# Kernel tuning notes

Hardware: AMD Instinct MI355X
Metric: run time of the kernel (lower is better)

## Reference

```python
import jax, jax.numpy as jnp
import numpy as np

SEQ, BATCH, IN, H = 2048, 1024, 10, 20


def setup_inputs() -> dict:
    key = jax.random.key(0)
    ks = jax.random.split(key, 11)
    s = 1.0 / np.sqrt(H)  # PyTorch LSTM init range
    u = lambda k, shape: jax.random.uniform(k, shape, jnp.float32, -s, s)
    return {
        "x": jax.random.normal(ks[0], (SEQ, BATCH, IN), jnp.float32),
        "h0": jax.random.normal(ks[1], (2, BATCH, H), jnp.float32),
        "c0": jax.random.normal(ks[2], (2, BATCH, H), jnp.float32),
        "w_ih_f": u(ks[3], (4 * H, IN)),
        "w_hh_f": u(ks[4], (4 * H, H)),
        "b_ih_f": u(ks[5], (4 * H,)),
        "b_hh_f": u(ks[6], (4 * H,)),
        "w_ih_b": u(ks[7], (4 * H, IN)),
        "w_hh_b": u(ks[8], (4 * H, H)),
        "b_ih_b": u(ks[9], (4 * H,)),
        "b_hh_b": u(ks[10], (4 * H,)),
    }


def _scan_dir(x_proj, h0, c0, w_hh):
    # x_proj: [seq, batch, 4H] precomputed input projection + biases
    def step(carry, g_in):
        h, c = carry
        g = g_in + h @ w_hh.T  # [batch, 4H]
        i, f, gg, o = jnp.split(g, 4, axis=-1)  # PyTorch gate order i,f,g,o
        c = jax.nn.sigmoid(f) * c + jax.nn.sigmoid(i) * jnp.tanh(gg)
        h = jax.nn.sigmoid(o) * jnp.tanh(c)
        return (h, c), h

    (hT, cT), hs = jax.lax.scan(step, (h0, c0), x_proj)
    return hs, hT, cT


def reference(x, h0, c0, w_ih_f, w_hh_f, b_ih_f, b_hh_f, w_ih_b, w_hh_b, b_ih_b, b_hh_b):
    # forward direction
    xf = jnp.einsum('sbi,gi->sbg', x, w_ih_f) + (b_ih_f + b_hh_f)
    hs_f, hT_f, cT_f = _scan_dir(xf, h0[0], c0[0], w_hh_f)
    # backward direction: scan over time-reversed sequence, then flip outputs
    xb = jnp.einsum('sbi,gi->sbg', x[::-1], w_ih_b) + (b_ih_b + b_hh_b)
    hs_b, hT_b, cT_b = _scan_dir(xb, h0[1], c0[1], w_hh_b)
    hs_b = hs_b[::-1]
    out = jnp.concatenate([hs_f, hs_b], axis=-1)  # [seq, batch, 2H]
    h_n = jnp.stack([hT_f, hT_b])  # [2, batch, H]
    c_n = jnp.stack([cT_f, cT_b])
    return out, h_n, c_n
```

## Files before the change

### kernel.cpp

```cpp
#include <hip/hip_runtime.h>

namespace {

constexpr int SEQ = 2048, BATCH = 1024, IN = 10, H = 20;
constexpr int XS  = 32;
constexpr int XRW = 8;
constexpr float L2E = 1.4426950408889634f;
constexpr float K2  = -2.0f * L2E;

typedef _Float16 h2t __attribute__((ext_vector_type(2)));

__device__ __forceinline__ float rcpf(float x) { return __builtin_amdgcn_rcpf(x); }
__device__ __forceinline__ float xp2(float x)  { return __builtin_amdgcn_exp2f(x); }

__device__ __forceinline__ int pk(float a, float b) {
    auto v = __builtin_amdgcn_cvt_pkrtz(a, b);
    int i; __builtin_memcpy(&i, &v, 4); return i;
}
__device__ __forceinline__ float dot2(int a, int b, float c) {
    h2t ha, hb; __builtin_memcpy(&ha, &a, 4); __builtin_memcpy(&hb, &b, 4);
    return __builtin_amdgcn_fdot2(ha, hb, c, false);
}
__device__ __forceinline__ float dpp_x1(float v) {
    int i; __builtin_memcpy(&i, &v, 4);
    int r = __builtin_amdgcn_update_dpp(0, i, 0xB1, 0xF, 0xF, true);
    float f; __builtin_memcpy(&f, &r, 4); return f;
}
__device__ __forceinline__ float dpp_x2(float v) {
    int i; __builtin_memcpy(&i, &v, 4);
    int r = __builtin_amdgcn_update_dpp(0, i, 0x4E, 0xF, 0xF, true);
    float f; __builtin_memcpy(&f, &r, 4); return f;
}

template<int DIR>
__device__ __forceinline__ void run_dir(const float* __restrict__ x,
                                        const float* __restrict__ h0,
                                        const float* __restrict__ c0,
                                        const float* __restrict__ w_ih,
                                        const float* __restrict__ w_hh,
                                        const float* __restrict__ bi,
                                        const float* __restrict__ bh,
                                        float* __restrict__ out,
                                        float* __restrict__ h_n,
                                        float* __restrict__ c_n,
                                        int b, int lane,
                                        int* xlds, int* hl)
{
    const int u    = lane >> 1;
    const int gp   = lane & 1;
    const int ur   = (u < H) ? u : (H - 1);
    const bool red = (gp == 0) && (u < H);

    const bool okp  = ((lane & 3) == 0) && (u < H);
    const int  hoff = okp ? (lane >> 2) : (16 + lane);

    const int g0 = gp * 2 * H + ur, g1 = g0 + H;
    const float sc0 = gp ? K2 : (-L2E);
    const float sc1 = -L2E;
    const float na0 = gp ? (2.0f * K2) : 1.0f;
    const float nd0 = gp ? (-K2) : 0.0f;

    int wh[2][10], wi[2][5]; float bias[2];
    #pragma unroll
    for (int k = 0; k < 10; ++k) {
        wh[0][k] = pk(w_hh[g0 * H + 2 * k] * sc0, w_hh[g0 * H + 2 * k + 1] * sc0);
        wh[1][k] = pk(w_hh[g1 * H + 2 * k] * sc1, w_hh[g1 * H + 2 * k + 1] * sc1);
    }
    #pragma unroll
    for (int k = 0; k < 5; ++k) {
        wi[0][k] = pk(w_ih[g0 * IN + 2 * k] * sc0, w_ih[g0 * IN + 2 * k + 1] * sc0);
        wi[1][k] = pk(w_ih[g1 * IN + 2 * k] * sc1, w_ih[g1 * IN + 2 * k + 1] * sc1);
    }
    bias[0] = (bi[g0] + bh[g0]) * sc0;
    bias[1] = (bi[g1] + bh[g1]) * sc1;

    float c  = c0[(DIR * BATCH + b) * H + ur] * K2;
    float hv = h0[(DIR * BATCH + b) * H + ur];

    hl[hoff] = pk(hv, dpp_x2(hv));

    constexpr ptrdiff_t XSTEP = DIR ? -(ptrdiff_t)(BATCH * IN) : (ptrdiff_t)(BATCH * IN);
    constexpr ptrdiff_t XOFF0 = DIR ? (ptrdiff_t)(SEQ - 1) * (BATCH * IN) : 0;
    const float* xbase = x + b * IN + XOFF0;

    float2 pend[3];
    auto issue_chunk = [&](int s0) {
        #pragma unroll
        for (int i = 0; i < 3; ++i) {
            const int e = lane + 64 * i;
            if (i < 2 || lane < 32) {
                const int ss = e / 5, j = e % 5;
                pend[i] = *(const float2*)(xbase + (ptrdiff_t)(s0 + ss) * XSTEP + 2 * j);
            }
        }
    };
    auto write_chunk = [&](int buf) {
        #pragma unroll
        for (int i = 0; i < 3; ++i) {
            const int e = lane + 64 * i;
            if (i < 2 || lane < 32)
                xlds[buf * (XS * XRW) + (e / 5) * XRW + (e % 5)] = pk(pend[i].x, pend[i].y);
        }
    };

    issue_chunk(0);  write_chunk(0);
    issue_chunk(XS);

    constexpr ptrdiff_t OSTEP  = DIR ? -(ptrdiff_t)(BATCH * 2 * H) : (ptrdiff_t)(BATCH * 2 * H);
    ptrdiff_t           orow   = DIR ? (ptrdiff_t)(SEQ - 1) * (BATCH * 2 * H) : 0;
    const int           oconst = b * (2 * H) + DIR * H + ur;

    for (int s0 = 0; s0 < SEQ; s0 += XS) {
        const int buf = (s0 >> 5) & 1;
        #pragma unroll 4
        for (int ss = 0; ss < XS; ++ss) {
            const int* xr = &xlds[buf * (XS * XRW) + ss * XRW];
            const int4 xA4 = *(const int4*)xr;
            const int  x4  = xr[4];
            const int  xq[5] = { xA4.x, xA4.y, xA4.z, xA4.w, x4 };

            const int4 h04 = *(const int4*)&hl[0];
            const int4 h48 = *(const int4*)&hl[4];
            const int2 h89 = *(const int2*)&hl[8];
            const int  hp[10] = { h04.x, h04.y, h04.z, h04.w,
                                  h48.x, h48.y, h48.z, h48.w, h89.x, h89.y };

            float a0 = bias[0], a1 = bias[1], p0 = 0.0f, p1 = 0.0f;
            #pragma unroll
            for (int k = 0; k < 3; ++k) {
                a0 = dot2(xq[k], wi[0][k], a0);
                a1 = dot2(xq[k], wi[1][k], a1);
            }
            #pragma unroll
            for (int k = 3; k < 5; ++k) {
                p0 = dot2(xq[k], wi[0][k], p0);
                p1 = dot2(xq[k], wi[1][k], p1);
            }
            #pragma unroll
            for (int k = 0; k < 5; ++k) {
                a0 = dot2(hp[k],     wh[0][k],     a0);
                a1 = dot2(hp[k],     wh[1][k],     a1);
                p0 = dot2(hp[k + 5], wh[0][k + 5], p0);
                p1 = dot2(hp[k + 5], wh[1][k + 5], p1);
            }
            a0 += p0;  a1 += p1;

            const float n0 = fmaf(na0, rcpf(1.0f + xp2(a0)), nd0);
            const float n1 = rcpf(1.0f + xp2(a1));

            const float m0 = dpp_x1(n0);
            const float m1 = dpp_x1(n1);
            const float F  = gp ? m1 : n1;
            c = fmaf(F, c, n0 * m0);
            const float th = fmaf(2.0f, rcpf(1.0f + xp2(c)), -1.0f);
            const float o  = gp ? n1 : m1;
            hv = o * th;

            const int pair = pk(hv, dpp_x2(hv));
            hl[hoff] = pair;
            if (red) __builtin_nontemporal_store(hv, out + orow + oconst);
            orow += OSTEP;
        }
        if (s0 + XS < SEQ) {
            write_chunk(buf ^ 1);
            if (s0 + 2 * XS < SEQ) issue_chunk(s0 + 2 * XS);
        }
    }

    if (red) {
        h_n[(DIR * BATCH + b) * H + ur] = hv;
        c_n[(DIR * BATCH + b) * H + ur] = c * (1.0f / K2);
    }
}

__launch_bounds__(64)
__global__ void lstm_bidir(const float* __restrict__ x,
                           const float* __restrict__ h0,
                           const float* __restrict__ c0,
                           const float* __restrict__ w_ih_f, const float* __restrict__ w_hh_f,
                           const float* __restrict__ b_ih_f, const float* __restrict__ b_hh_f,
                           const float* __restrict__ w_ih_b, const float* __restrict__ w_hh_b,
                           const float* __restrict__ b_ih_b, const float* __restrict__ b_hh_b,
                           float* __restrict__ out, float* __restrict__ h_n, float* __restrict__ c_n)
{
    __shared__ __align__(16) int xlds[2 * XS * XRW];
    __shared__ __align__(16) int hl[80];

    const int b    = blockIdx.x;
    const int lane = threadIdx.x;

    if (blockIdx.y == 0)
        run_dir<0>(x, h0, c0, w_ih_f, w_hh_f, b_ih_f, b_hh_f, out, h_n, c_n, b, lane, xlds, hl);
    else
        run_dir<1>(x, h0, c0, w_ih_b, w_hh_b, b_ih_b, b_hh_b, out, h_n, c_n, b, lane, xlds, hl);
}

}

extern "C" void kernel_launch(void* const* d_in, const int* in_sizes, int n_in,
                              void* d_out, int out_size, void* d_ws, size_t ws_size,
                              hipStream_t stream)
{
    const float* x      = (const float*)d_in[0];
    const float* h0     = (const float*)d_in[1];
    const float* c0     = (const float*)d_in[2];
    const float* w_ih_f = (const float*)d_in[3];
    const float* w_hh_f = (const float*)d_in[4];
    const float* b_ih_f = (const float*)d_in[5];
    const float* b_hh_f = (const float*)d_in[6];
    const float* w_ih_b = (const float*)d_in[7];
    const float* w_hh_b = (const float*)d_in[8];
    const float* b_ih_b = (const float*)d_in[9];
    const float* b_hh_b = (const float*)d_in[10];

    float* out = (float*)d_out;
    float* h_n = out + (size_t)SEQ * BATCH * 2 * H;
    float* c_n = h_n + (size_t)2 * BATCH * H;

    dim3 grid(BATCH, 2), block(64);
    hipLaunchKernelGGL(lstm_bidir, grid, block, 0, stream,
                       x, h0, c0, w_ih_f, w_hh_f, b_ih_f, b_hh_f,
                       w_ih_b, w_hh_b, b_ih_b, b_hh_b, out, h_n, c_n);
}
```

Baseline: 585.8 us.

## Process two batch rows per wavefront with one hidden unit per lane

Remaps work so each 64-lane wavefront handles two batch elements, with 20 lanes per element each computing all four gates of one hidden unit. This replaces the earlier split of gates across lane pairs and removes the DPP exchanges between them, and it halves the grid. The next step's x operands are now read from LDS one step ahead. Each lane now does twice the dot products per step and holds more weight registers, and the serial per-step chain gets longer.

```diff
diff --git a/kernel.cpp b/kernel.cpp
--- a/kernel.cpp
+++ b/kernel.cpp
@@ -4,7 +4,7 @@
 
 constexpr int SEQ = 2048, BATCH = 1024, IN = 10, H = 20;
 constexpr int XS  = 32;
-constexpr int XRW = 8;
+constexpr int XRW = 16;
 constexpr float L2E = 1.4426950408889634f;
 constexpr float K2  = -2.0f * L2E;
 
@@ -12,6 +12,7 @@
 
 __device__ __forceinline__ float rcpf(float x) { return __builtin_amdgcn_rcpf(x); }
 __device__ __forceinline__ float xp2(float x)  { return __builtin_amdgcn_exp2f(x); }
+__device__ __forceinline__ float sig2(float a) { return rcpf(1.0f + xp2(a)); }
 
 __device__ __forceinline__ int pk(float a, float b) {
     auto v = __builtin_amdgcn_cvt_pkrtz(a, b);
@@ -24,11 +25,6 @@
 __device__ __forceinline__ float dpp_x1(float v) {
     int i; __builtin_memcpy(&i, &v, 4);
     int r = __builtin_amdgcn_update_dpp(0, i, 0xB1, 0xF, 0xF, true);
-    float f; __builtin_memcpy(&f, &r, 4); return f;
-}
-__device__ __forceinline__ float dpp_x2(float v) {
-    int i; __builtin_memcpy(&i, &v, 4);
-    int r = __builtin_amdgcn_update_dpp(0, i, 0x4E, 0xF, 0xF, true);
     float f; __builtin_memcpy(&f, &r, 4); return f;
 }
 
@@ -43,133 +39,134 @@
                                         float* __restrict__ out,
                                         float* __restrict__ h_n,
                                         float* __restrict__ c_n,
-                                        int b, int lane,
+                                        int b2, int lane,
                                         int* xlds, int* hl)
 {
-    const int u    = lane >> 1;
-    const int gp   = lane & 1;
-    const int ur   = (u < H) ? u : (H - 1);
-    const bool red = (gp == 0) && (u < H);
-
-    const bool okp  = ((lane & 3) == 0) && (u < H);
-    const int  hoff = okp ? (lane >> 2) : (16 + lane);
-
-    const int g0 = gp * 2 * H + ur, g1 = g0 + H;
-    const float sc0 = gp ? K2 : (-L2E);
-    const float sc1 = -L2E;
-    const float na0 = gp ? (2.0f * K2) : 1.0f;
-    const float nd0 = gp ? (-K2) : 0.0f;
-
-    int wh[2][10], wi[2][5]; float bias[2];
+    const int  c    = lane / 20;
+    const int  u    = lane % 20;
+    const int  cc   = (c < 2) ? c : 1;
+    const bool act  = (c < 2);
+    const int  bgl  = 2 * b2 + cc;
+
+    const bool okp  = act && ((u & 1) == 0);
+    const int  offH = okp ? (cc * 16 + (u >> 1)) : (32 + lane);
+
+    int wh[4][10], wi[4][5]; float bias[4];
     #pragma unroll
-    for (int k = 0; k < 10; ++k) {
-        wh[0][k] = pk(w_hh[g0 * H + 2 * k] * sc0, w_hh[g0 * H + 2 * k + 1] * sc0);
-        wh[1][k] = pk(w_hh[g1 * H + 2 * k] * sc1, w_hh[g1 * H + 2 * k + 1] * sc1);
+    for (int q = 0; q < 4; ++q) {
+        const float sc = (q == 2) ? K2 : (-L2E);
+        const int g = q * H + u;
+        #pragma unroll
+        for (int k = 0; k < 10; ++k)
+            wh[q][k] = pk(w_hh[g * H + 2 * k] * sc, w_hh[g * H + 2 * k + 1] * sc);
+        #pragma unroll
+        for (int k = 0; k < 5; ++k)
+            wi[q][k] = pk(w_ih[g * IN + 2 * k] * sc, w_ih[g * IN + 2 * k + 1] * sc);
+        bias[q] = (bi[g] + bh[g]) * sc;
     }
-    #pragma unroll
-    for (int k = 0; k < 5; ++k) {
-        wi[0][k] = pk(w_ih[g0 * IN + 2 * k] * sc0, w_ih[g0 * IN + 2 * k + 1] * sc0);
-        wi[1][k] = pk(w_ih[g1 * IN + 2 * k] * sc1, w_ih[g1 * IN + 2 * k + 1] * sc1);
-    }
-    bias[0] = (bi[g0] + bh[g0]) * sc0;
-    bias[1] = (bi[g1] + bh[g1]) * sc1;
-
-    float c  = c0[(DIR * BATCH + b) * H + ur] * K2;
-    float hv = h0[(DIR * BATCH + b) * H + ur];
-
-    hl[hoff] = pk(hv, dpp_x2(hv));
+
+    float cv = c0[(DIR * BATCH + bgl) * H + u] * K2;
+    float hv = h0[(DIR * BATCH + bgl) * H + u];
 
     constexpr ptrdiff_t XSTEP = DIR ? -(ptrdiff_t)(BATCH * IN) : (ptrdiff_t)(BATCH * IN);
     constexpr ptrdiff_t XOFF0 = DIR ? (ptrdiff_t)(SEQ - 1) * (BATCH * IN) : 0;
-    const float* xbase = x + b * IN + XOFF0;
-
-    float2 pend[3];
+    const float* xbase = x + (2 * b2) * IN + XOFF0;
+
+    float2 pend[5];
     auto issue_chunk = [&](int s0) {
         #pragma unroll
-        for (int i = 0; i < 3; ++i) {
+        for (int i = 0; i < 5; ++i) {
             const int e = lane + 64 * i;
-            if (i < 2 || lane < 32) {
-                const int ss = e / 5, j = e % 5;
-                pend[i] = *(const float2*)(xbase + (ptrdiff_t)(s0 + ss) * XSTEP + 2 * j);
-            }
+            pend[i] = *(const float2*)(xbase + (ptrdiff_t)(s0 + e / 10) * XSTEP + 2 * (e % 10));
         }
     };
     auto write_chunk = [&](int buf) {
         #pragma unroll
-        for (int i = 0; i < 3; ++i) {
+        for (int i = 0; i < 5; ++i) {
             const int e = lane + 64 * i;
-            if (i < 2 || lane < 32)
-                xlds[buf * (XS * XRW) + (e / 5) * XRW + (e % 5)] = pk(pend[i].x, pend[i].y);
-        }
+            const int j = e % 10;
+            xlds[buf * (XS * XRW) + (e / 10) * XRW + j + (j >= 5 ? 3 : 0)] = pk(pend[i].x, pend[i].y);
+        }
+    };
+    auto read_x = [&](int buf, int ss, int (&xq)[5]) {
+        const int* xr = &xlds[buf * (XS * XRW) + ss * XRW + cc * 8];
+        const int4 xa = *(const int4*)xr;
+        xq[0] = xa.x; xq[1] = xa.y; xq[2] = xa.z; xq[3] = xa.w; xq[4] = xr[4];
+    };
+    auto read_h = [&](int (&hp)[10]) {
+        const int* hr = &hl[cc * 16];
+        const int4 hA = *(const int4*)hr;
+        const int4 hB = *(const int4*)(hr + 4);
+        const int2 hC = *(const int2*)(hr + 8);
+        hp[0]=hA.x; hp[1]=hA.y; hp[2]=hA.z; hp[3]=hA.w;
+        hp[4]=hB.x; hp[5]=hB.y; hp[6]=hB.z; hp[7]=hB.w;
+        hp[8]=hC.x; hp[9]=hC.y;
     };
 
     issue_chunk(0);  write_chunk(0);
     issue_chunk(XS);
 
-    constexpr ptrdiff_t OSTEP  = DIR ? -(ptrdiff_t)(BATCH * 2 * H) : (ptrdiff_t)(BATCH * 2 * H);
-    ptrdiff_t           orow   = DIR ? (ptrdiff_t)(SEQ - 1) * (BATCH * 2 * H) : 0;
-    const int           oconst = b * (2 * H) + DIR * H + ur;
+    hl[offH] = pk(hv, dpp_x1(hv));
+    int hp[10], xq[5];
+    read_h(hp);
+    read_x(0, 0, xq);
+
+    constexpr ptrdiff_t OSTEP = DIR ? -(ptrdiff_t)(BATCH * 2 * H) : (ptrdiff_t)(BATCH * 2 * H);
+    ptrdiff_t           orow  = DIR ? (ptrdiff_t)(SEQ - 1) * (BATCH * 2 * H) : 0;
+    const int           ocst  = bgl * (2 * H) + DIR * H + u;
 
     for (int s0 = 0; s0 < SEQ; s0 += XS) {
         const int buf = (s0 >> 5) & 1;
         #pragma unroll 4
         for (int ss = 0; ss < XS; ++ss) {
-            const int* xr = &xlds[buf * (XS * XRW) + ss * XRW];
-            const int4 xA4 = *(const int4*)xr;
-            const int  x4  = xr[4];
-            const int  xq[5] = { xA4.x, xA4.y, xA4.z, xA4.w, x4 };
-
-            const int4 h04 = *(const int4*)&hl[0];
-            const int4 h48 = *(const int4*)&hl[4];
-            const int2 h89 = *(const int2*)&hl[8];
-            const int  hp[10] = { h04.x, h04.y, h04.z, h04.w,
-                                  h48.x, h48.y, h48.z, h48.w, h89.x, h89.y };
-
-            float a0 = bias[0], a1 = bias[1], p0 = 0.0f, p1 = 0.0f;
+            int xqn[5];
+            if (ss < XS - 1) read_x(buf, ss + 1, xqn);
+
+            float a0 = bias[0], a1 = bias[1], a2 = bias[2], a3 = bias[3];
             #pragma unroll
-            for (int k = 0; k < 3; ++k) {
+            for (int k = 0; k < 5; ++k) {
                 a0 = dot2(xq[k], wi[0][k], a0);
                 a1 = dot2(xq[k], wi[1][k], a1);
+                a2 = dot2(xq[k], wi[2][k], a2);
+                a3 = dot2(xq[k], wi[3][k], a3);
             }
             #pragma unroll
-            for (int k = 3; k < 5; ++k) {
-                p0 = dot2(xq[k], wi[0][k], p0);
-                p1 = dot2(xq[k], wi[1][k], p1);
+            for (int k = 0; k < 10; ++k) {
+                a0 = dot2(hp[k], wh[0][k], a0);
+                a1 = dot2(hp[k], wh[1][k], a1);
+                a2 = dot2(hp[k], wh[2][k], a2);
+                a3 = dot2(hp[k], wh[3][k], a3);
             }
-            #pragma unroll
-            for (int k = 0; k < 5; ++k) {
-                a0 = dot2(hp[k],     wh[0][k],     a0);
-                a1 = dot2(hp[k],     wh[1][k],     a1);
-                p0 = dot2(hp[k + 5], wh[0][k + 5], p0);
-                p1 = dot2(hp[k + 5], wh[1][k + 5], p1);
+
+            const float si = sig2(a0);
+            const float sf = sig2(a1);
+            const float n2 = fmaf(2.0f * K2, sig2(a2), -K2);
+            const float so = sig2(a3);
+            cv = fmaf(sf, cv, si * n2);
+            const float th = fmaf(2.0f, sig2(cv), -1.0f);
+            hv = so * th;
+
+            hl[offH] = pk(hv, dpp_x1(hv));
+            read_h(hp);
+
+            if (act) __builtin_nontemporal_store(hv, out + orow + ocst);
+            orow += OSTEP;
+
+            if (ss < XS - 1) {
+                #pragma unroll
+                for (int k = 0; k < 5; ++k) xq[k] = xqn[k];
             }
-            a0 += p0;  a1 += p1;
-
-            const float n0 = fmaf(na0, rcpf(1.0f + xp2(a0)), nd0);
-            const float n1 = rcpf(1.0f + xp2(a1));
-
-            const float m0 = dpp_x1(n0);
-            const float m1 = dpp_x1(n1);
-            const float F  = gp ? m1 : n1;
-            c = fmaf(F, c, n0 * m0);
-            const float th = fmaf(2.0f, rcpf(1.0f + xp2(c)), -1.0f);
-            const float o  = gp ? n1 : m1;
-            hv = o * th;
-
-            const int pair = pk(hv, dpp_x2(hv));
-            hl[hoff] = pair;
-            if (red) __builtin_nontemporal_store(hv, out + orow + oconst);
-            orow += OSTEP;
         }
         if (s0 + XS < SEQ) {
             write_chunk(buf ^ 1);
             if (s0 + 2 * XS < SEQ) issue_chunk(s0 + 2 * XS);
+            read_x(buf ^ 1, 0, xq);
         }
     }
 
-    if (red) {
-        h_n[(DIR * BATCH + b) * H + ur] = hv;
-        c_n[(DIR * BATCH + b) * H + ur] = c * (1.0f / K2);
+    if (act) {
+        h_n[(DIR * BATCH + bgl) * H + u] = hv;
+        c_n[(DIR * BATCH + bgl) * H + u] = cv * (1.0f / K2);
     }
 }
 
@@ -184,15 +181,15 @@
                            float* __restrict__ out, float* __restrict__ h_n, float* __restrict__ c_n)
 {
     __shared__ __align__(16) int xlds[2 * XS * XRW];
-    __shared__ __align__(16) int hl[80];
-
-    const int b    = blockIdx.x;
+    __shared__ __align__(16) int hl[96];
+
+    const int b2   = blockIdx.x;
     const int lane = threadIdx.x;
 
     if (blockIdx.y == 0)
-        run_dir<0>(x, h0, c0, w_ih_f, w_hh_f, b_ih_f, b_hh_f, out, h_n, c_n, b, lane, xlds, hl);
+        run_dir<0>(x, h0, c0, w_ih_f, w_hh_f, b_ih_f, b_hh_f, out, h_n, c_n, b2, lane, xlds, hl);
     else
-        run_dir<1>(x, h0, c0, w_ih_b, w_hh_b, b_ih_b, b_hh_b, out, h_n, c_n, b, lane, xlds, hl);
+        run_dir<1>(x, h0, c0, w_ih_b, w_hh_b, b_ih_b, b_hh_b, out, h_n, c_n, b2, lane, xlds, hl);
 }
 
 }
@@ -217,7 +214,7 @@
     float* h_n = out + (size_t)SEQ * BATCH * 2 * H;
     float* c_n = h_n + (size_t)2 * BATCH * H;
 
-    dim3 grid(BATCH, 2), block(64);
+    dim3 grid(BATCH / 2, 2), block(64);
     hipLaunchKernelGGL(lstm_bidir, grid, block, 0, stream,
                        x, h0, c0, w_ih_f, w_hh_f, b_ih_f, b_hh_f,
                        w_ih_b, w_hh_b, b_ih_b, b_hh_b, out, h_n, c_n);
```

New measurement: 497.1 us. -15.1%, faster.
